# Optimization experiments

Measured on AMD Instinct MI355X. Metric: run time of the kernel, lower is better.

Reference implementation:

```python
import jax, jax.numpy as jnp
import numpy as np

EPSILON = 1000000000.0
N_HEADS = 8
N_UNITS = 512
D_K = N_UNITS // N_HEADS  # 64
B, S = 2, 2048


def setup_inputs() -> dict:
    key = jax.random.key(0)
    ks = jax.random.split(key, 12)
    k_init = 1.0 / np.sqrt(N_UNITS)
    u = lambda k, shape: jax.random.uniform(k, shape, jnp.float32, -k_init, k_init)
    return {
        "query": jax.random.normal(ks[0], (B, S, N_UNITS), jnp.float32),
        "key": jax.random.normal(ks[1], (B, S, N_UNITS), jnp.float32),
        "value": jax.random.normal(ks[2], (B, S, N_UNITS), jnp.float32),
        "mask": jnp.ones((B, S, S), jnp.float32),
        # Stacked per-head projection weights, [H, D, d_k] (x @ W), biases [H, d_k]
        "Wq": u(ks[3], (N_HEADS, N_UNITS, D_K)),
        "bq": u(ks[4], (N_HEADS, D_K)),
        "Wk": u(ks[5], (N_HEADS, N_UNITS, D_K)),
        "bk": u(ks[6], (N_HEADS, D_K)),
        "Wv": u(ks[7], (N_HEADS, N_UNITS, D_K)),
        "bv": u(ks[8], (N_HEADS, D_K)),
        # Output projection: x @ Wo + bo, Wo [D, D]
        "Wo": u(ks[9], (N_UNITS, N_UNITS)),
        "bo": u(ks[10], (N_UNITS,)),
    }


def reference(query, key, value, mask, Wq, bq, Wk, bk, Wv, bv, Wo, bo):
    # Batched over heads: q/k/v projections -> [B, H, S, d_k]
    q = jnp.einsum("bsd,hdk->bhsk", query, Wq) + bq[None, :, None, :]
    k = jnp.einsum("bsd,hdk->bhsk", key, Wk) + bk[None, :, None, :]
    v = jnp.einsum("bsd,hdk->bhsk", value, Wv) + bv[None, :, None, :]
    # Scaled dot-product scores [B, H, S, S]
    scores = jnp.einsum("bhsk,bhtk->bhst", q, k) / jnp.sqrt(jnp.asarray(D_K, q.dtype))
    # Additive masking exactly as original: x*mask - EPS*(1-mask)
    m = mask[:, None, :, :]
    scores = scores * m - EPSILON * (1.0 - m)
    a = jax.nn.softmax(scores, axis=-1)
    ctx = jnp.einsum("bhst,bhtk->bhsk", a, v)  # [B, H, S, d_k]
    # Concatenate heads along feature dim -> [B, S, H*d_k]
    h_out = ctx.transpose(0, 2, 1, 3).reshape(query.shape[0], query.shape[1], N_UNITS)
    return h_out @ Wo + bo
```

## Files before the change

### kernel.cpp

```cpp
#include <hip/hip_runtime.h>
#include <hip/hip_bf16.h>


#define DEVI __device__ __forceinline__

typedef float f32x4 __attribute__((ext_vector_type(4)));
typedef __bf16 bf16x8 __attribute__((ext_vector_type(8)));

constexpr int S  = 2048;
constexpr int D  = 512;
constexpr int H  = 8;
constexpr int DK = 64;
constexpr int BATCH = 2;
constexpr int BS = BATCH * S;

DEVI unsigned short f2bf(float f) {
  union { float f; unsigned u; } v; v.f = f;
  unsigned r = v.u + 0x7fffu + ((v.u >> 16) & 1u);
  return (unsigned short)(r >> 16);
}

DEVI f32x4 mfma16(bf16x8 a, bf16x8 b, f32x4 c) {
  return __builtin_amdgcn_mfma_f32_16x16x32_bf16(a, b, c, 0, 0, 0);
}

DEVI bf16x8 ldg8(const unsigned short* p) { return *(const bf16x8*)p; }

__global__ __launch_bounds__(256) void prep_w_kernel(
    const float* __restrict__ Wq, const float* __restrict__ Wk,
    const float* __restrict__ Wv, const float* __restrict__ Wo,
    unsigned short* __restrict__ Wt)
{
  __shared__ float T[64][65];
  int bid = blockIdx.x;
  int g = bid >> 6, t = bid & 63;
  int tn = t >> 3, td = t & 7;
  int n0 = tn * 64, d0 = td * 64;
  int tid = threadIdx.x;
  const float* src = (g == 0) ? Wq : (g == 1) ? Wk : (g == 2) ? Wv : Wo;

  #pragma unroll
  for (int cc = 0; cc < 4; ++cc) {
    int id = tid + cc * 256;
    int dd = id >> 4, f4 = (id & 15) * 4;
    const float* p = (g < 3)
      ? src + ((size_t)tn * D + d0 + dd) * DK + f4
      : src + (size_t)(d0 + dd) * D + n0 + f4;
    float4 x = *(const float4*)p;
    T[dd][f4 + 0] = x.x; T[dd][f4 + 1] = x.y;
    T[dd][f4 + 2] = x.z; T[dd][f4 + 3] = x.w;
  }
  __syncthreads();

  #pragma unroll
  for (int cc = 0; cc < 2; ++cc) {
    int id = tid + cc * 256;
    int nn = id >> 3, ch = (id & 7) * 8;
    unsigned short o8[8];
    #pragma unroll
    for (int j = 0; j < 8; ++j) o8[j] = f2bf(T[ch + j][nn]);
    *(uint4*)&Wt[((size_t)g * D + n0 + nn) * D + d0 + ch] = *(const uint4*)o8;
  }
}

__global__ __launch_bounds__(256) void proj_qkv_kernel(
    const float* __restrict__ query, const float* __restrict__ key,
    const float* __restrict__ value, const unsigned short* __restrict__ Wt,
    const float* __restrict__ bq, const float* __restrict__ bk, const float* __restrict__ bv,
    unsigned short* __restrict__ Qb, unsigned short* __restrict__ Kb,
    unsigned short* __restrict__ Vtb)
{
  int z = blockIdx.z;
  const float* A = (z == 0) ? query : (z == 1) ? key : value;
  const unsigned short* Bt = Wt + (size_t)z * D * D;
  const float* bias = (z == 0) ? bq : (z == 1) ? bk : bv;

  __shared__ __align__(16) unsigned short At[128][72];
  __shared__ __align__(16) unsigned short Btile[128][72];

  int tid = threadIdx.x;
  int w = tid >> 6, l = tid & 63;
  int g = l >> 4, c = l & 15;
  int wm = w >> 1, wn = w & 1;
  int m0 = blockIdx.y * 128, n0 = blockIdx.x * 128;

  f32x4 acc[4][4];
  #pragma unroll
  for (int i = 0; i < 4; ++i)
    #pragma unroll
    for (int j = 0; j < 4; ++j) acc[i][j] = f32x4{0.f, 0.f, 0.f, 0.f};

  for (int k0 = 0; k0 < D; k0 += 64) {
    __syncthreads();
    #pragma unroll
    for (int cc = 0; cc < 4; ++cc) {
      int id = tid + cc * 256;
      int row = id >> 3, ch = (id & 7) * 8;
      const float* p = A + (size_t)(m0 + row) * D + k0 + ch;
      float4 x0 = *(const float4*)p, x1 = *(const float4*)(p + 4);
      unsigned short o8[8] = { f2bf(x0.x), f2bf(x0.y), f2bf(x0.z), f2bf(x0.w),
                               f2bf(x1.x), f2bf(x1.y), f2bf(x1.z), f2bf(x1.w) };
      *(uint4*)&At[row][ch] = *(const uint4*)o8;
      *(bf16x8*)&Btile[row][ch] = ldg8(Bt + (size_t)(n0 + row) * D + k0 + ch);
    }
    __syncthreads();
    #pragma unroll
    for (int dc = 0; dc < 2; ++dc) {
      bf16x8 af[4], bv4[4];
      #pragma unroll
      for (int i = 0; i < 4; ++i)
        af[i] = *(const bf16x8*)&At[wm * 64 + i * 16 + c][dc * 32 + 8 * g];
      #pragma unroll
      for (int j = 0; j < 4; ++j)
        bv4[j] = *(const bf16x8*)&Btile[wn * 64 + j * 16 + c][dc * 32 + 8 * g];
      #pragma unroll
      for (int i = 0; i < 4; ++i)
        #pragma unroll
        for (int j = 0; j < 4; ++j)
          acc[i][j] = mfma16(af[i], bv4[j], acc[i][j]);
    }
  }

  #pragma unroll
  for (int i = 0; i < 4; ++i) {
    #pragma unroll
    for (int j = 0; j < 4; ++j) {
      int col = n0 + wn * 64 + j * 16 + c;
      float bb = bias[col];
      #pragma unroll
      for (int r = 0; r < 4; ++r) {
        int m = m0 + wm * 64 + i * 16 + 4 * g + r;
        unsigned short o = f2bf(acc[i][j][r] + bb);
        if (z == 0)      Qb[(size_t)m * D + col] = o;
        else if (z == 1) Kb[(size_t)m * D + col] = o;
        else {
          int b_ = m >> 11, s_ = m & 2047;
          Vtb[((size_t)b_ * D + col) * S + s_] = o;
        }
      }
    }
  }
}

__global__ __launch_bounds__(256) void proj_o_kernel(
    const unsigned short* __restrict__ Ctx, const unsigned short* __restrict__ Bt,
    const float* __restrict__ bo, float* __restrict__ out)
{
  __shared__ __align__(16) unsigned short At[128][72];
  __shared__ __align__(16) unsigned short Btile[128][72];

  int tid = threadIdx.x;
  int w = tid >> 6, l = tid & 63;
  int g = l >> 4, c = l & 15;
  int wm = w >> 1, wn = w & 1;
  int m0 = blockIdx.y * 128, n0 = blockIdx.x * 128;

  f32x4 acc[4][4];
  #pragma unroll
  for (int i = 0; i < 4; ++i)
    #pragma unroll
    for (int j = 0; j < 4; ++j) acc[i][j] = f32x4{0.f, 0.f, 0.f, 0.f};

  for (int k0 = 0; k0 < D; k0 += 64) {
    __syncthreads();
    #pragma unroll
    for (int cc = 0; cc < 4; ++cc) {
      int id = tid + cc * 256;
      int row = id >> 3, ch = (id & 7) * 8;
      *(bf16x8*)&At[row][ch]    = ldg8(Ctx + (size_t)(m0 + row) * D + k0 + ch);
      *(bf16x8*)&Btile[row][ch] = ldg8(Bt  + (size_t)(n0 + row) * D + k0 + ch);
    }
    __syncthreads();
    #pragma unroll
    for (int dc = 0; dc < 2; ++dc) {
      bf16x8 af[4], bv4[4];
      #pragma unroll
      for (int i = 0; i < 4; ++i)
        af[i] = *(const bf16x8*)&At[wm * 64 + i * 16 + c][dc * 32 + 8 * g];
      #pragma unroll
      for (int j = 0; j < 4; ++j)
        bv4[j] = *(const bf16x8*)&Btile[wn * 64 + j * 16 + c][dc * 32 + 8 * g];
      #pragma unroll
      for (int i = 0; i < 4; ++i)
        #pragma unroll
        for (int j = 0; j < 4; ++j)
          acc[i][j] = mfma16(af[i], bv4[j], acc[i][j]);
    }
  }

  #pragma unroll
  for (int i = 0; i < 4; ++i) {
    #pragma unroll
    for (int j = 0; j < 4; ++j) {
      int col = n0 + wn * 64 + j * 16 + c;
      float bb = bo[col];
      #pragma unroll
      for (int r = 0; r < 4; ++r) {
        int m = m0 + wm * 64 + i * 16 + 4 * g + r;
        out[(size_t)m * D + col] = acc[i][j][r] + bb;
      }
    }
  }
}

__global__ __launch_bounds__(256) void attn_kernel(
    const unsigned short* __restrict__ Qb, const unsigned short* __restrict__ Kb,
    const unsigned short* __restrict__ Vtb, const float* __restrict__ mask,
    unsigned short* __restrict__ Ctx)
{
  __shared__ __align__(16) unsigned short Kt[64][72];
  __shared__ __align__(16) unsigned short Vt[64][72];
  __shared__ __align__(16) unsigned short Pl[4][16][72];

  int tid = threadIdx.x;
  int w = tid >> 6, l = tid & 63;
  int g = l >> 4, c = l & 15;
  int bh = blockIdx.y, b = bh >> 3, h = bh & 7;
  int q0 = blockIdx.x * 64 + w * 16;

  bf16x8 qf[2];
  #pragma unroll
  for (int dc = 0; dc < 2; ++dc)
    qf[dc] = ldg8(Qb + (size_t)(b * S + q0 + c) * D + h * DK + dc * 32 + 8 * g);

  float m_run[4], l_run[4];
  f32x4 o_acc[4];
  #pragma unroll
  for (int r = 0; r < 4; ++r) { m_run[r] = -1e30f; l_run[r] = 0.f; }
  #pragma unroll
  for (int nf = 0; nf < 4; ++nf) o_acc[nf] = f32x4{0.f, 0.f, 0.f, 0.f};

  for (int kb = 0; kb < S; kb += 64) {
    __syncthreads();
    #pragma unroll
    for (int cc = 0; cc < 2; ++cc) {
      int id = tid + cc * 256;
      int row = id >> 3, ch = (id & 7) * 8;
      *(bf16x8*)&Kt[row][ch] = ldg8(Kb + (size_t)(b * S + kb + row) * D + h * DK + ch);
      *(bf16x8*)&Vt[row][ch] = ldg8(Vtb + ((size_t)bh * DK + row) * S + kb + ch);
    }
    __syncthreads();

    f32x4 sacc[4];
    #pragma unroll
    for (int fc = 0; fc < 4; ++fc) sacc[fc] = f32x4{0.f, 0.f, 0.f, 0.f};
    #pragma unroll
    for (int fc = 0; fc < 4; ++fc)
      #pragma unroll
      for (int dc = 0; dc < 2; ++dc) {
        bf16x8 kf = *(const bf16x8*)&Kt[fc * 16 + c][dc * 32 + 8 * g];
        sacc[fc] = mfma16(qf[dc], kf, sacc[fc]);
      }

    float p[4][4], mx[4];
    #pragma unroll
    for (int r = 0; r < 4; ++r) mx[r] = -1e30f;
    #pragma unroll
    for (int fc = 0; fc < 4; ++fc)
      #pragma unroll
      for (int r = 0; r < 4; ++r) {
        int qrow = q0 + 4 * g + r;
        float mv = mask[((size_t)b * S + qrow) * S + kb + fc * 16 + c];
        float sv = sacc[fc][r] * 0.125f;
        sv = sv * mv - 1e9f * (1.0f - mv);
        p[fc][r] = sv;
        mx[r] = fmaxf(mx[r], sv);
      }
    #pragma unroll
    for (int r = 0; r < 4; ++r) {
      float v = mx[r];
      v = fmaxf(v, __shfl_xor(v, 1, 64));
      v = fmaxf(v, __shfl_xor(v, 2, 64));
      v = fmaxf(v, __shfl_xor(v, 4, 64));
      v = fmaxf(v, __shfl_xor(v, 8, 64));
      float mnew = fmaxf(m_run[r], v);
      float corr = exp2f((m_run[r] - mnew) * 1.44269504f);
      m_run[r] = mnew;
      float rs = 0.f;
      #pragma unroll
      for (int fc = 0; fc < 4; ++fc) {
        float pe = exp2f((p[fc][r] - mnew) * 1.44269504f);
        p[fc][r] = pe;
        rs += pe;
      }
      rs += __shfl_xor(rs, 1, 64);
      rs += __shfl_xor(rs, 2, 64);
      rs += __shfl_xor(rs, 4, 64);
      rs += __shfl_xor(rs, 8, 64);
      l_run[r] = l_run[r] * corr + rs;
      #pragma unroll
      for (int nf = 0; nf < 4; ++nf) o_acc[nf][r] *= corr;
      #pragma unroll
      for (int fc = 0; fc < 4; ++fc)
        Pl[w][4 * g + r][fc * 16 + c] = f2bf(p[fc][r]);
    }

    #pragma unroll
    for (int kc = 0; kc < 2; ++kc) {
      bf16x8 vf[4];
      #pragma unroll
      for (int nf = 0; nf < 4; ++nf)
        vf[nf] = *(const bf16x8*)&Vt[nf * 16 + c][kc * 32 + 8 * g];
      bf16x8 pf = *(const bf16x8*)&Pl[w][c][kc * 32 + 8 * g];
      #pragma unroll
      for (int nf = 0; nf < 4; ++nf)
        o_acc[nf] = mfma16(pf, vf[nf], o_acc[nf]);
    }
  }

  #pragma unroll
  for (int r = 0; r < 4; ++r) {
    float inv = 1.0f / l_run[r];
    int qrow = q0 + 4 * g + r;
    #pragma unroll
    for (int nf = 0; nf < 4; ++nf)
      Ctx[((size_t)b * S + qrow) * D + h * DK + nf * 16 + c] = f2bf(o_acc[nf][r] * inv);
  }
}

extern "C" void kernel_launch(void* const* d_in, const int* in_sizes, int n_in,
                              void* d_out, int out_size, void* d_ws, size_t ws_size,
                              hipStream_t stream) {
  (void)in_sizes; (void)n_in; (void)out_size; (void)ws_size;
  const float* query = (const float*)d_in[0];
  const float* key   = (const float*)d_in[1];
  const float* value = (const float*)d_in[2];
  const float* mask  = (const float*)d_in[3];
  const float* Wq    = (const float*)d_in[4];
  const float* bq    = (const float*)d_in[5];
  const float* Wk    = (const float*)d_in[6];
  const float* bk    = (const float*)d_in[7];
  const float* Wv    = (const float*)d_in[8];
  const float* bv    = (const float*)d_in[9];
  const float* Wo    = (const float*)d_in[10];
  const float* bo    = (const float*)d_in[11];
  float* out = (float*)d_out;

  char* ws = (char*)d_ws;
  unsigned short* Wt  = (unsigned short*)(ws);
  unsigned short* Qb  = (unsigned short*)(ws + 2097152);
  unsigned short* Kb  = (unsigned short*)(ws + 6291456);
  unsigned short* Vtb = (unsigned short*)(ws + 10485760);
  unsigned short* Ctx = (unsigned short*)(ws + 14680064);

  hipLaunchKernelGGL(prep_w_kernel, dim3(256), dim3(256), 0, stream,
                     Wq, Wk, Wv, Wo, Wt);
  hipLaunchKernelGGL(proj_qkv_kernel, dim3(4, 32, 3), dim3(256), 0, stream,
                     query, key, value, Wt, bq, bk, bv, Qb, Kb, Vtb);
  hipLaunchKernelGGL(attn_kernel, dim3(32, 16), dim3(256), 0, stream,
                     Qb, Kb, Vtb, mask, Ctx);
  hipLaunchKernelGGL(proj_o_kernel, dim3(4, 32), dim3(256), 0, stream,
                     Ctx, Wt + 3 * D * D, bo, out);
}
```

Before: 223.6 us.

## Rewrite attention with 32x32 MFMA, register P reuse, and swizzled LDS

The attention kernel now uses 32x32x16 bf16 MFMA with 32 queries per wave. K and V tiles sit in XOR-swizzled LDS, mask rows are read as float4, and the P matrix is repacked in registers with cross-half shuffles instead of a round trip through LDS. The softmax scale and log2e are folded into Q in the projection epilogue. V is transposed through LDS so Vt is written with coalesced stores, and the output projection moves to 64x64 tiles to launch more blocks. Together these aim to cut LDS traffic, shuffle reductions and uncoalesced global writes, at the risk of more register pressure and subtle layout bugs in the P repacking.

```diff
diff --git a/kernel.cpp b/kernel.cpp
--- a/kernel.cpp
+++ b/kernel.cpp
@@ -5,6 +5,7 @@
 #define DEVI __device__ __forceinline__
 
 typedef float f32x4 __attribute__((ext_vector_type(4)));
+typedef float f32x16 __attribute__((ext_vector_type(16)));
 typedef __bf16 bf16x8 __attribute__((ext_vector_type(8)));
 
 constexpr int S  = 2048;
@@ -14,14 +15,24 @@
 constexpr int BATCH = 2;
 constexpr int BS = BATCH * S;
 
+constexpr float SCALE_QK = 0.18033688011112433f;
+constexpr float EPS2     = 1.4426950408889634e9f;
+
 DEVI unsigned short f2bf(float f) {
   union { float f; unsigned u; } v; v.f = f;
   unsigned r = v.u + 0x7fffu + ((v.u >> 16) & 1u);
   return (unsigned short)(r >> 16);
 }
 
+DEVI unsigned pk2(float a, float b) {
+  return (unsigned)f2bf(a) | ((unsigned)f2bf(b) << 16);
+}
+
 DEVI f32x4 mfma16(bf16x8 a, bf16x8 b, f32x4 c) {
   return __builtin_amdgcn_mfma_f32_16x16x32_bf16(a, b, c, 0, 0, 0);
+}
+DEVI f32x16 mfma32(bf16x8 a, bf16x8 b, f32x16 c) {
+  return __builtin_amdgcn_mfma_f32_32x32x16_bf16(a, b, c, 0, 0, 0);
 }
 
 DEVI bf16x8 ldg8(const unsigned short* p) { return *(const bf16x8*)p; }
@@ -75,8 +86,9 @@
   const unsigned short* Bt = Wt + (size_t)z * D * D;
   const float* bias = (z == 0) ? bq : (z == 1) ? bk : bv;
 
-  __shared__ __align__(16) unsigned short At[128][72];
-  __shared__ __align__(16) unsigned short Btile[128][72];
+  __shared__ __align__(16) unsigned short SM[2 * 128 * 72];
+  unsigned short (*At)[72]    = (unsigned short(*)[72])SM;
+  unsigned short (*Btile)[72] = (unsigned short(*)[72])(SM + 128 * 72);
 
   int tid = threadIdx.x;
   int w = tid >> 6, l = tid & 63;
@@ -121,23 +133,47 @@
     }
   }
 
-  #pragma unroll
-  for (int i = 0; i < 4; ++i) {
-    #pragma unroll
-    for (int j = 0; j < 4; ++j) {
-      int col = n0 + wn * 64 + j * 16 + c;
-      float bb = bias[col];
-      #pragma unroll
-      for (int r = 0; r < 4; ++r) {
-        int m = m0 + wm * 64 + i * 16 + 4 * g + r;
-        unsigned short o = f2bf(acc[i][j][r] + bb);
-        if (z == 0)      Qb[(size_t)m * D + col] = o;
-        else if (z == 1) Kb[(size_t)m * D + col] = o;
-        else {
-          int b_ = m >> 11, s_ = m & 2047;
-          Vtb[((size_t)b_ * D + col) * S + s_] = o;
+  if (z < 2) {
+    #pragma unroll
+    for (int i = 0; i < 4; ++i) {
+      #pragma unroll
+      for (int j = 0; j < 4; ++j) {
+        int col = n0 + wn * 64 + j * 16 + c;
+        float bb = bias[col];
+        #pragma unroll
+        for (int r = 0; r < 4; ++r) {
+          int m = m0 + wm * 64 + i * 16 + 4 * g + r;
+          float vv = acc[i][j][r] + bb;
+          if (z == 0) vv *= SCALE_QK;
+          unsigned short o = f2bf(vv);
+          if (z == 0) Qb[(size_t)m * D + col] = o;
+          else        Kb[(size_t)m * D + col] = o;
         }
       }
+    }
+  } else {
+    __syncthreads();
+    unsigned short (*Vl)[130] = (unsigned short(*)[130])SM;
+    #pragma unroll
+    for (int i = 0; i < 4; ++i)
+      #pragma unroll
+      for (int j = 0; j < 4; ++j) {
+        int col = wn * 64 + j * 16 + c;
+        float bb = bias[n0 + col];
+        #pragma unroll
+        for (int r = 0; r < 4; ++r)
+          Vl[wm * 64 + i * 16 + 4 * g + r][col] = f2bf(acc[i][j][r] + bb);
+      }
+    __syncthreads();
+    int b_ = m0 >> 11, s0b = m0 & 2047;
+    #pragma unroll
+    for (int it = 0; it < 8; ++it) {
+      int id = tid + it * 256;
+      int nl = id >> 4, chm = (id & 15) * 8;
+      unsigned short o8[8];
+      #pragma unroll
+      for (int jj = 0; jj < 8; ++jj) o8[jj] = Vl[chm + jj][nl];
+      *(uint4*)(Vtb + ((size_t)b_ * D + n0 + nl) * S + s0b + chm) = *(const uint4*)o8;
     }
   }
 }
@@ -146,25 +182,25 @@
     const unsigned short* __restrict__ Ctx, const unsigned short* __restrict__ Bt,
     const float* __restrict__ bo, float* __restrict__ out)
 {
-  __shared__ __align__(16) unsigned short At[128][72];
-  __shared__ __align__(16) unsigned short Btile[128][72];
+  __shared__ __align__(16) unsigned short At[64][72];
+  __shared__ __align__(16) unsigned short Btile[64][72];
 
   int tid = threadIdx.x;
   int w = tid >> 6, l = tid & 63;
   int g = l >> 4, c = l & 15;
   int wm = w >> 1, wn = w & 1;
-  int m0 = blockIdx.y * 128, n0 = blockIdx.x * 128;
-
-  f32x4 acc[4][4];
-  #pragma unroll
-  for (int i = 0; i < 4; ++i)
-    #pragma unroll
-    for (int j = 0; j < 4; ++j) acc[i][j] = f32x4{0.f, 0.f, 0.f, 0.f};
+  int m0 = blockIdx.y * 64, n0 = blockIdx.x * 64;
+
+  f32x4 acc[2][2];
+  #pragma unroll
+  for (int i = 0; i < 2; ++i)
+    #pragma unroll
+    for (int j = 0; j < 2; ++j) acc[i][j] = f32x4{0.f, 0.f, 0.f, 0.f};
 
   for (int k0 = 0; k0 < D; k0 += 64) {
     __syncthreads();
     #pragma unroll
-    for (int cc = 0; cc < 4; ++cc) {
+    for (int cc = 0; cc < 2; ++cc) {
       int id = tid + cc * 256;
       int row = id >> 3, ch = (id & 7) * 8;
       *(bf16x8*)&At[row][ch]    = ldg8(Ctx + (size_t)(m0 + row) * D + k0 + ch);
@@ -173,34 +209,33 @@
     __syncthreads();
     #pragma unroll
     for (int dc = 0; dc < 2; ++dc) {
-      bf16x8 af[4], bv4[4];
-      #pragma unroll
-      for (int i = 0; i < 4; ++i)
-        af[i] = *(const bf16x8*)&At[wm * 64 + i * 16 + c][dc * 32 + 8 * g];
-      #pragma unroll
-      for (int j = 0; j < 4; ++j)
-        bv4[j] = *(const bf16x8*)&Btile[wn * 64 + j * 16 + c][dc * 32 + 8 * g];
-      #pragma unroll
-      for (int i = 0; i < 4; ++i)
+      bf16x8 af[2], bv4[2];
+      #pragma unroll
+      for (int i = 0; i < 2; ++i)
+        af[i] = *(const bf16x8*)&At[wm * 32 + i * 16 + c][dc * 32 + 8 * g];
+      #pragma unroll
+      for (int j = 0; j < 2; ++j)
+        bv4[j] = *(const bf16x8*)&Btile[wn * 32 + j * 16 + c][dc * 32 + 8 * g];
+      #pragma unroll
+      for (int i = 0; i < 2; ++i)
         #pragma unroll
-        for (int j = 0; j < 4; ++j)
+        for (int j = 0; j < 2; ++j)
           acc[i][j] = mfma16(af[i], bv4[j], acc[i][j]);
     }
   }
 
   #pragma unroll
-  for (int i = 0; i < 4; ++i) {
-    #pragma unroll
-    for (int j = 0; j < 4; ++j) {
-      int col = n0 + wn * 64 + j * 16 + c;
+  for (int i = 0; i < 2; ++i)
+    #pragma unroll
+    for (int j = 0; j < 2; ++j) {
+      int col = n0 + wn * 32 + j * 16 + c;
       float bb = bo[col];
       #pragma unroll
       for (int r = 0; r < 4; ++r) {
-        int m = m0 + wm * 64 + i * 16 + 4 * g + r;
+        int m = m0 + wm * 32 + i * 16 + 4 * g + r;
         out[(size_t)m * D + col] = acc[i][j][r] + bb;
       }
     }
-  }
 }
 
 __global__ __launch_bounds__(256) void attn_kernel(
@@ -208,113 +243,148 @@
     const unsigned short* __restrict__ Vtb, const float* __restrict__ mask,
     unsigned short* __restrict__ Ctx)
 {
-  __shared__ __align__(16) unsigned short Kt[64][72];
-  __shared__ __align__(16) unsigned short Vt[64][72];
-  __shared__ __align__(16) unsigned short Pl[4][16][72];
+  __shared__ __align__(16) unsigned short Kt[64 * 64];
+  __shared__ __align__(16) unsigned short Vt[64 * 64];
+  __shared__ __align__(16) unsigned short Ol[4][32][72];
 
   int tid = threadIdx.x;
-  int w = tid >> 6, l = tid & 63;
-  int g = l >> 4, c = l & 15;
+  int wid = tid >> 6, l = tid & 63;
+  int ql = l & 31, half = l >> 5;
   int bh = blockIdx.y, b = bh >> 3, h = bh & 7;
-  int q0 = blockIdx.x * 64 + w * 16;
-
-  bf16x8 qf[2];
-  #pragma unroll
-  for (int dc = 0; dc < 2; ++dc)
-    qf[dc] = ldg8(Qb + (size_t)(b * S + q0 + c) * D + h * DK + dc * 32 + 8 * g);
-
-  float m_run[4], l_run[4];
-  f32x4 o_acc[4];
-  #pragma unroll
-  for (int r = 0; r < 4; ++r) { m_run[r] = -1e30f; l_run[r] = 0.f; }
-  #pragma unroll
-  for (int nf = 0; nf < 4; ++nf) o_acc[nf] = f32x4{0.f, 0.f, 0.f, 0.f};
+  int q0 = blockIdx.x * 128 + wid * 32;
+  int q = q0 + ql;
+
+  bf16x8 qf[4];
+  #pragma unroll
+  for (int t = 0; t < 4; ++t)
+    qf[t] = ldg8(Qb + (size_t)(b * S + q) * D + h * DK + t * 16 + half * 8);
+
+  float m_run = -1e30f, l_run = 0.f;
+  f32x16 o0, o1;
+  #pragma unroll
+  for (int i = 0; i < 16; ++i) { o0[i] = 0.f; o1[i] = 0.f; }
 
   for (int kb = 0; kb < S; kb += 64) {
     __syncthreads();
     #pragma unroll
-    for (int cc = 0; cc < 2; ++cc) {
-      int id = tid + cc * 256;
-      int row = id >> 3, ch = (id & 7) * 8;
-      *(bf16x8*)&Kt[row][ch] = ldg8(Kb + (size_t)(b * S + kb + row) * D + h * DK + ch);
-      *(bf16x8*)&Vt[row][ch] = ldg8(Vtb + ((size_t)bh * DK + row) * S + kb + ch);
-    }
-    __syncthreads();
-
-    f32x4 sacc[4];
-    #pragma unroll
-    for (int fc = 0; fc < 4; ++fc) sacc[fc] = f32x4{0.f, 0.f, 0.f, 0.f};
-    #pragma unroll
-    for (int fc = 0; fc < 4; ++fc)
-      #pragma unroll
-      for (int dc = 0; dc < 2; ++dc) {
-        bf16x8 kf = *(const bf16x8*)&Kt[fc * 16 + c][dc * 32 + 8 * g];
-        sacc[fc] = mfma16(qf[dc], kf, sacc[fc]);
-      }
-
-    float p[4][4], mx[4];
-    #pragma unroll
-    for (int r = 0; r < 4; ++r) mx[r] = -1e30f;
-    #pragma unroll
-    for (int fc = 0; fc < 4; ++fc)
-      #pragma unroll
-      for (int r = 0; r < 4; ++r) {
-        int qrow = q0 + 4 * g + r;
-        float mv = mask[((size_t)b * S + qrow) * S + kb + fc * 16 + c];
-        float sv = sacc[fc][r] * 0.125f;
-        sv = sv * mv - 1e9f * (1.0f - mv);
-        p[fc][r] = sv;
-        mx[r] = fmaxf(mx[r], sv);
-      }
-    #pragma unroll
-    for (int r = 0; r < 4; ++r) {
-      float v = mx[r];
-      v = fmaxf(v, __shfl_xor(v, 1, 64));
-      v = fmaxf(v, __shfl_xor(v, 2, 64));
-      v = fmaxf(v, __shfl_xor(v, 4, 64));
-      v = fmaxf(v, __shfl_xor(v, 8, 64));
-      float mnew = fmaxf(m_run[r], v);
-      float corr = exp2f((m_run[r] - mnew) * 1.44269504f);
-      m_run[r] = mnew;
-      float rs = 0.f;
-      #pragma unroll
-      for (int fc = 0; fc < 4; ++fc) {
-        float pe = exp2f((p[fc][r] - mnew) * 1.44269504f);
-        p[fc][r] = pe;
+    for (int it = 0; it < 2; ++it) {
+      int id = tid + it * 256;
+      int row = id >> 3, ch = id & 7;
+      int sw = ((ch * 16) ^ ((row & 7) << 4)) >> 1;
+      *(bf16x8*)(Kt + row * 64 + sw) =
+          ldg8(Kb + (size_t)(b * S + kb + row) * D + h * DK + ch * 8);
+      *(bf16x8*)(Vt + row * 64 + sw) =
+          ldg8(Vtb + ((size_t)b * D + h * DK + row) * S + kb + ch * 8);
+    }
+    __syncthreads();
+
+    f32x16 s0, s1;
+    #pragma unroll
+    for (int i = 0; i < 16; ++i) { s0[i] = 0.f; s1[i] = 0.f; }
+    #pragma unroll
+    for (int t = 0; t < 4; ++t) {
+      int cb = ((t * 32 + half * 16) ^ ((ql & 7) << 4)) >> 1;
+      bf16x8 k0 = *(const bf16x8*)(Kt + ql * 64 + cb);
+      bf16x8 k1 = *(const bf16x8*)(Kt + (32 + ql) * 64 + cb);
+      s0 = mfma32(k0, qf[t], s0);
+      s1 = mfma32(k1, qf[t], s1);
+    }
+
+    float y[2][16];
+    const float* mrow = mask + ((size_t)b * S + q) * S + kb;
+    #pragma unroll
+    for (int ks = 0; ks < 2; ++ks)
+      #pragma unroll
+      for (int rg = 0; rg < 4; ++rg) {
+        float4 mv = *(const float4*)(mrow + ks * 32 + rg * 8 + half * 4);
+        float sv0 = ks ? s1[rg * 4 + 0] : s0[rg * 4 + 0];
+        float sv1 = ks ? s1[rg * 4 + 1] : s0[rg * 4 + 1];
+        float sv2 = ks ? s1[rg * 4 + 2] : s0[rg * 4 + 2];
+        float sv3 = ks ? s1[rg * 4 + 3] : s0[rg * 4 + 3];
+        y[ks][rg * 4 + 0] = fmaf(sv0, mv.x, fmaf(EPS2, mv.x, -EPS2));
+        y[ks][rg * 4 + 1] = fmaf(sv1, mv.y, fmaf(EPS2, mv.y, -EPS2));
+        y[ks][rg * 4 + 2] = fmaf(sv2, mv.z, fmaf(EPS2, mv.z, -EPS2));
+        y[ks][rg * 4 + 3] = fmaf(sv3, mv.w, fmaf(EPS2, mv.w, -EPS2));
+      }
+
+    float mx = -1e30f;
+    #pragma unroll
+    for (int ks = 0; ks < 2; ++ks)
+      #pragma unroll
+      for (int i = 0; i < 16; ++i) mx = fmaxf(mx, y[ks][i]);
+    mx = fmaxf(mx, __shfl_xor(mx, 32, 64));
+    float mnew = fmaxf(m_run, mx);
+    float corr = exp2f(m_run - mnew);
+    m_run = mnew;
+
+    float p[2][16];
+    float rs = 0.f;
+    #pragma unroll
+    for (int ks = 0; ks < 2; ++ks)
+      #pragma unroll
+      for (int i = 0; i < 16; ++i) {
+        float pe = exp2f(y[ks][i] - mnew);
+        p[ks][i] = pe;
         rs += pe;
       }
-      rs += __shfl_xor(rs, 1, 64);
-      rs += __shfl_xor(rs, 2, 64);
-      rs += __shfl_xor(rs, 4, 64);
-      rs += __shfl_xor(rs, 8, 64);
-      l_run[r] = l_run[r] * corr + rs;
-      #pragma unroll
-      for (int nf = 0; nf < 4; ++nf) o_acc[nf][r] *= corr;
-      #pragma unroll
-      for (int fc = 0; fc < 4; ++fc)
-        Pl[w][4 * g + r][fc * 16 + c] = f2bf(p[fc][r]);
-    }
-
-    #pragma unroll
-    for (int kc = 0; kc < 2; ++kc) {
-      bf16x8 vf[4];
-      #pragma unroll
-      for (int nf = 0; nf < 4; ++nf)
-        vf[nf] = *(const bf16x8*)&Vt[nf * 16 + c][kc * 32 + 8 * g];
-      bf16x8 pf = *(const bf16x8*)&Pl[w][c][kc * 32 + 8 * g];
-      #pragma unroll
-      for (int nf = 0; nf < 4; ++nf)
-        o_acc[nf] = mfma16(pf, vf[nf], o_acc[nf]);
-    }
-  }
-
-  #pragma unroll
-  for (int r = 0; r < 4; ++r) {
-    float inv = 1.0f / l_run[r];
-    int qrow = q0 + 4 * g + r;
-    #pragma unroll
-    for (int nf = 0; nf < 4; ++nf)
-      Ctx[((size_t)b * S + qrow) * D + h * DK + nf * 16 + c] = f2bf(o_acc[nf][r] * inv);
+    rs += __shfl_xor(rs, 32, 64);
+    l_run = l_run * corr + rs;
+    o0 = o0 * corr;
+    o1 = o1 * corr;
+
+    unsigned w[2][4][2], xw[2][4][2];
+    #pragma unroll
+    for (int ks = 0; ks < 2; ++ks)
+      #pragma unroll
+      for (int rg = 0; rg < 4; ++rg) {
+        w[ks][rg][0] = pk2(p[ks][rg * 4 + 0], p[ks][rg * 4 + 1]);
+        w[ks][rg][1] = pk2(p[ks][rg * 4 + 2], p[ks][rg * 4 + 3]);
+      }
+    #pragma unroll
+    for (int ks = 0; ks < 2; ++ks)
+      #pragma unroll
+      for (int rg = 0; rg < 4; ++rg) {
+        xw[ks][rg][0] = (unsigned)__shfl_xor((int)w[ks][rg][0], 32, 64);
+        xw[ks][rg][1] = (unsigned)__shfl_xor((int)w[ks][rg][1], 32, 64);
+      }
+
+    bf16x8 pa[4];
+    #pragma unroll
+    for (int ks = 0; ks < 2; ++ks)
+      #pragma unroll
+      for (int sub = 0; sub < 2; ++sub) {
+        unsigned u0 = half ? xw[ks][2 * sub + 1][0] : w[ks][2 * sub][0];
+        unsigned u1 = half ? xw[ks][2 * sub + 1][1] : w[ks][2 * sub][1];
+        unsigned u2 = half ? w[ks][2 * sub + 1][0]  : xw[ks][2 * sub][0];
+        unsigned u3 = half ? w[ks][2 * sub + 1][1]  : xw[ks][2 * sub][1];
+        union { unsigned u[4]; bf16x8 v; } pu;
+        pu.u[0] = u0; pu.u[1] = u1; pu.u[2] = u2; pu.u[3] = u3;
+        pa[ks * 2 + sub] = pu.v;
+      }
+
+    #pragma unroll
+    for (int kp = 0; kp < 4; ++kp) {
+      int cb = ((kp * 32 + half * 16) ^ ((ql & 7) << 4)) >> 1;
+      bf16x8 v0 = *(const bf16x8*)(Vt + ql * 64 + cb);
+      bf16x8 v1 = *(const bf16x8*)(Vt + (32 + ql) * 64 + cb);
+      o0 = mfma32(v0, pa[kp], o0);
+      o1 = mfma32(v1, pa[kp], o1);
+    }
+  }
+
+  float inv = 1.0f / l_run;
+  #pragma unroll
+  for (int i = 0; i < 16; ++i) {
+    int dr = (i & 3) + 8 * (i >> 2) + 4 * half;
+    Ol[wid][ql][dr]      = f2bf(o0[i] * inv);
+    Ol[wid][ql][32 + dr] = f2bf(o1[i] * inv);
+  }
+  #pragma unroll
+  for (int it = 0; it < 4; ++it) {
+    int id = l + it * 64;
+    int row = id >> 3, ch = (id & 7) * 8;
+    bf16x8 vv = *(const bf16x8*)&Ol[wid][row][ch];
+    *(bf16x8*)(Ctx + (size_t)(b * S + q0 + row) * D + h * DK + ch) = vv;
   }
 }
 
@@ -347,8 +417,8 @@
                      Wq, Wk, Wv, Wo, Wt);
   hipLaunchKernelGGL(proj_qkv_kernel, dim3(4, 32, 3), dim3(256), 0, stream,
                      query, key, value, Wt, bq, bk, bv, Qb, Kb, Vtb);
-  hipLaunchKernelGGL(attn_kernel, dim3(32, 16), dim3(256), 0, stream,
+  hipLaunchKernelGGL(attn_kernel, dim3(16, 16), dim3(256), 0, stream,
                      Qb, Kb, Vtb, mask, Ctx);
-  hipLaunchKernelGGL(proj_o_kernel, dim3(4, 32), dim3(256), 0, stream,
+  hipLaunchKernelGGL(proj_o_kernel, dim3(8, 64), dim3(256), 0, stream,
                      Ctx, Wt + 3 * D * D, bo, out);
 }
```

After: 232.9 us. 4.1% more time.
